# Optimization experiments

Hardware: AMD Instinct MI355X
Metric: run time of the kernel (lower is better)

The kernel has to match this reference:

```python
import jax, jax.numpy as jnp
import numpy as np

CAL = {
 'x': (-0.0025095, 0.0022181),
 'onnxMatMul_166': (-0.22075387835502625, 0.208940327167511),
 'fc1MatMul': (-0.00291599917, 0.0017367251),
 'fc1bias': (-0.48688140511512756, 0.5176185369491577),
 'fc1Add': (-0.48778465390205383, 0.5181604027748108),
 'Wiz_1': (-0.43284985423088074, 0.46175122261047363),
 'Wir_1': (-0.34401071071624756, 0.29191476106643677),
 'Win_1': (-0.3236880302429199, 0.39607325196266174),
 'Whz_1': (-1.8417714834213257, 1.7173254489898682),
 'Whr_1': (-1.1574513912200928, 1.0300449132919312),
 'Whn_1': (-0.7756922245025635, 0.9530389308929443),
 'biz_1': (-0.5063393712043762, 0.36664387583732605),
 'bir_1': (-0.07920225709676743, 0.20611026883125305),
 'bin_1': (-0.5539973378181458, 0.17938342690467834),
 'bhz_1': (-0.5337516665458679, 0.4148772358894348),
 'bhr_1': (-0.07688436657190323, 0.14814253151416779),
 'bhn_1': (-0.7828555107116699, 0.9008108973503113),
 'Wiz_2': (-0.9102030992507935, 0.9408696889877319),
 'Wir_2': (-0.9560997486114502, 0.6683358550071716),
 'Win_2': (-0.4721935987472534, 0.48561596870422363),
 'Whz_2': (-1.2992678880691528, 1.2991048097610474),
 'Whr_2': (-0.8318714499473572, 1.1085889339447021),
 'Whn_2': (-0.955470085144043, 1.046797513961792),
 'biz_2': (-0.44805487990379333, 0.1560053527355194),
 'bir_2': (-0.08767592161893845, 0.11347303539514542),
 'bin_2': (-0.239909827709198, 0.12033259868621826),
 'bhz_2': (-0.43745461106300354, 0.12699371576309204),
 'bhr_2': (-0.09617264568805695, 0.07690174877643585),
 'bhn_2': (-0.17204178869724274, 0.19739042222499847),
 'onnxMatMul_207': (-1.3657219409942627, 1.158295750617981),
 'fc2bias': (-0.1750922054052353, 0.1385071724653244),
 'onnxMatMul_208': (-3.1666038036346436, 2.5026357173919678),
 'fc3bias': (-0.10188056528568268, 0.0899151861667633),
 'onnxMatMul_209': (-1.300571084022522, 1.928941249847412),
 'fc4bias': (-0.10699586570262909, 0.04597663879394531),
 'h1': (-0.002647488145157695, 0.0028339680284261703),
 'h2': (-0.0031016061548143625, 0.0030250486452132463),
 'gru1_a_': (-0.6389939785003662, 0.7715625762939453),
 'gru1_a': (-0.6046768426895142, 0.8871182203292847),
 'gru1_b_': (-0.004922409541904926, 0.004103424027562141),
 'gru1_b': (-0.07475128024816513, 0.14630259573459625),
 'gru1_c_': (-1.5660111904144287, 1.0454494953155518),
 'gru1_c': (-1.9779117107391357, 1.3700535297393799),
 'gru1_d_': (-0.008429044857621193, 0.006403823848813772),
 'gru1_d': (-0.5529640316963196, 0.41507571935653687),
 'gru1_e_': (-1.3637111186981201, 1.018247127532959),
 'gru1_e': (-1.8583884239196777, 1.1587692499160767),
 'gru1_f_': (-0.005411399528384209, 0.0061536869034171104),
 'gru1_f': (-0.7833794355392456, 0.8978855013847351),
 'gru1_r_': (-0.6226556301116943, 0.9800534844398499),
 'gru1_r': (0.3491777181625366, 0.7271188497543335),
 'gru1_z_': (-2.392332077026367, 1.7851293087005615),
 'gru1_z': (0.08375928550958633, 0.856329083442688),
 'gru1_n1': (-0.5516456365585327, 0.4556601643562317),
 'gru1_n2': (-2.4100341796875, 1.1423156261444092),
 'gru1_n': (-0.983996570110321, 0.8151924014091492),
 'gru1_hn1': (0.143670916557312, 0.9162406921386719),
 'gru1_hn2': (-0.9015777111053467, 0.45391541719436646),
 'gru1_hn3': (-0.0016954239690676332, 0.0016671211924403906),
 'rnn1GRU': (-0.9016271829605103, 0.4546271562576294),
 'gru2_a_': (-0.681461751461029, 0.9113116264343262),
 'gru2_a': (-0.7149235010147095, 0.908741295337677),
 'gru2_b_': (-0.005148397758603096, 0.011014967225492),
 'gru2_b': (-0.09436552226543427, 0.07623167335987091),
 'gru2_c_': (-1.2279887199401855, 1.1102137565612793),
 'gru2_c': (-1.6760436296463013, 1.200895071029663),
 'gru2_d_': (-0.008141756057739258, 0.00894666276872158),
 'gru2_d': (-0.43875735998153687, 0.1262134611606598),
 'gru2_e_': (-0.6732944250106812, 0.6314664483070374),
}
# calib entries for gru2 past 'e_' were truncated in the source; reuse gru1 ranges
for _k in ['e', 'f_', 'f', 'r_', 'r', 'z_', 'z', 'n1', 'n2', 'n', 'hn1', 'hn2', 'hn3']:
    CAL.setdefault('gru2_' + _k, CAL['gru1_' + _k])
CAL['rnn2GRU'] = CAL['rnn1GRU']


def fq(x, name):
    """Per-tensor unsigned 8-bit fake-quantize/dequantize (CalibrationParam S/Z)."""
    mn, mx = CAL[name]
    s = (mx - mn) / 255.0  # 2**8 - 1
    z = float(round(-mn / s))
    q = jnp.clip(jnp.round(x / s) + z, 0.0, 255.0)
    y = (q - z) * s
    # straight-through: forward value is exact fake-quant, identity gradient
    return x + jax.lax.stop_gradient(y - x)


def _gru_layer(xs, Wiz, Wir, Win, Whz, Whr, Whn, biz, bir, binn, bhz, bhr, bhn, L):
    p = 'gru%d' % L
    Wiz = fq(Wiz, 'Wiz_%d' % L); Wir = fq(Wir, 'Wir_%d' % L); Win = fq(Win, 'Win_%d' % L)
    Whz = fq(Whz, 'Whz_%d' % L); Whr = fq(Whr, 'Whr_%d' % L); Whn = fq(Whn, 'Whn_%d' % L)
    biz = fq(biz, 'biz_%d' % L); bir = fq(bir, 'bir_%d' % L); binn = fq(binn, 'bin_%d' % L)
    bhz = fq(bhz, 'bhz_%d' % L); bhr = fq(bhr, 'bhr_%d' % L); bhn = fq(bhn, 'bhn_%d' % L)
    # input projections batched over all timesteps (xs: [T,B,H] time-major)
    A = fq(fq(jnp.einsum('tbi,ih->tbh', xs, Wir), p + '_a_') + bir, p + '_a')
    C = fq(fq(jnp.einsum('tbi,ih->tbh', xs, Wiz), p + '_c_') + biz, p + '_c')
    E = fq(fq(jnp.einsum('tbi,ih->tbh', xs, Win), p + '_e_') + binn, p + '_e')
    h0 = fq(jnp.zeros((xs.shape[1], Whz.shape[0]), xs.dtype), 'h%d' % L)

    def step(h, ace):
        a, c, e = ace
        b = fq(fq(h @ Whr, p + '_b_') + bhr, p + '_b')
        r = fq(jax.nn.sigmoid(fq(a + b, p + '_r_')), p + '_r')
        d = fq(fq(h @ Whz, p + '_d_') + bhz, p + '_d')
        z = fq(jax.nn.sigmoid(fq(c + d, p + '_z_')), p + '_z')
        f = fq(fq(h @ Whn, p + '_f_') + bhn, p + '_f')
        n = fq(jnp.tanh(fq(e + fq(r * f, p + '_n1'), p + '_n2')), p + '_n')
        hn2 = fq(fq(1.0 - z, p + '_hn1') * n, p + '_hn2')
        hn3 = fq(z * h, p + '_hn3')
        h_new = fq(hn2 + hn3, 'rnn%dGRU' % L)
        return h_new, h_new

    _, hs = jax.lax.scan(step, h0, (A, C, E))
    return hs


def setup_inputs() -> dict:
    B, T, F, H, D = 64, 1000, 257, 400, 600
    ks = iter(jax.random.split(jax.random.key(0), 64))

    def u(shape, name):
        mn, mx = CAL[name]
        return jax.random.uniform(next(ks), shape, jnp.float32, mn, mx)

    inp = {}
    inp['x'] = jax.random.normal(next(ks), (B, T, F), jnp.float32) * 0.001
    inp['W_fc1'] = u((F, H), 'onnxMatMul_166')
    inp['b_fc1'] = u((H,), 'fc1bias')
    for L in (1, 2):
        for g in ('z', 'r', 'n'):
            inp['Wi%s%d' % (g, L)] = u((H, H), 'Wi%s_%d' % (g, L))
            inp['Wh%s%d' % (g, L)] = u((H, H), 'Wh%s_%d' % (g, L))
            inp['bi%s%d' % (g, L)] = u((H,), 'bi%s_%d' % (g, L))
            inp['bh%s%d' % (g, L)] = u((H,), 'bh%s_%d' % (g, L))
    inp['W_fc2'] = u((H, D), 'onnxMatMul_207'); inp['b_fc2'] = u((D,), 'fc2bias')
    inp['W_fc3'] = u((D, D), 'onnxMatMul_208'); inp['b_fc3'] = u((D,), 'fc3bias')
    inp['W_fc4'] = u((D, F), 'onnxMatMul_209'); inp['b_fc4'] = u((F,), 'fc4bias')
    return inp


def reference(x, W_fc1, b_fc1, Wiz1, Wir1, Win1, Whz1, Whr1, Whn1, biz1, bir1, bin1, bhz1, bhr1, bhn1, Wiz2, Wir2, Win2, Whz2, Whr2, Whn2, biz2, bir2, bin2, bhz2, bhr2, bhn2, W_fc2, b_fc2, W_fc3, b_fc3, W_fc4, b_fc4):
    xq = fq(x, 'x')
    t = fq(jnp.einsum('bti,ih->bth', xq, fq(W_fc1, 'onnxMatMul_166')), 'fc1MatMul')
    t = fq(t + fq(b_fc1, 'fc1bias'), 'fc1Add')
    xs = jnp.swapaxes(t, 0, 1)  # [T,B,400]
    h1 = _gru_layer(xs, Wiz1, Wir1, Win1, Whz1, Whr1, Whn1, biz1, bir1, bin1, bhz1, bhr1, bhn1, 1)
    h2 = _gru_layer(h1, Wiz2, Wir2, Win2, Whz2, Whr2, Whn2, biz2, bir2, bin2, bhz2, bhr2, bhn2, 2)
    y = jnp.swapaxes(h2, 0, 1)  # [B,T,400]
    y = jax.nn.relu(jnp.einsum('bth,hd->btd', y, fq(W_fc2, 'onnxMatMul_207')) + fq(b_fc2, 'fc2bias'))
    y = jax.nn.relu(jnp.einsum('btd,de->bte', y, fq(W_fc3, 'onnxMatMul_208')) + fq(b_fc3, 'fc3bias'))
    y = jax.nn.sigmoid(jnp.einsum('bte,ef->btf', y, fq(W_fc4, 'onnxMatMul_209')) + fq(b_fc4, 'fc4bias'))
    return y
```

## Files before the change

### kernel.cpp

```cpp
#include <hip/hip_runtime.h>
#include <math.h>

#define DEV static __device__ __forceinline__

typedef int v4i __attribute__((ext_vector_type(4)));

struct SZ { float s, z; };

constexpr double cfloor_(double v){ long long i=(long long)v; return ((double)i > v) ? (double)(i-1) : (double)i; }
constexpr double cround_(double v){
  double fl = cfloor_(v); double fr = v - fl;
  return (fr > 0.5) ? fl + 1.0 : (fr < 0.5 ? fl : ((((long long)fl) & 1LL) == 0 ? fl : fl + 1.0));
}
constexpr SZ mksz(double mn, double mx){
  double s = (mx - mn) / 255.0;
  double z = cround_(-mn / s);
  return SZ{ (float)s, (float)z };
}

constexpr SZ Zx     = mksz(-0.0025095, 0.0022181);
constexpr SZ ZW1    = mksz(-0.22075387835502625, 0.208940327167511);
constexpr SZ Zfc1mm = mksz(-0.00291599917, 0.0017367251);
constexpr SZ Zbfc1  = mksz(-0.48688140511512756, 0.5176185369491577);
constexpr SZ Zfc1add= mksz(-0.48778465390205383, 0.5181604027748108);
constexpr SZ ZWiz1 = mksz(-0.43284985423088074, 0.46175122261047363);
constexpr SZ ZWir1 = mksz(-0.34401071071624756, 0.29191476106643677);
constexpr SZ ZWin1 = mksz(-0.3236880302429199, 0.39607325196266174);
constexpr SZ ZWhz1 = mksz(-1.8417714834213257, 1.7173254489898682);
constexpr SZ ZWhr1 = mksz(-1.1574513912200928, 1.0300449132919312);
constexpr SZ ZWhn1 = mksz(-0.7756922245025635, 0.9530389308929443);
constexpr SZ Zbiz1 = mksz(-0.5063393712043762, 0.36664387583732605);
constexpr SZ Zbir1 = mksz(-0.07920225709676743, 0.20611026883125305);
constexpr SZ Zbin1 = mksz(-0.5539973378181458, 0.17938342690467834);
constexpr SZ Zbhz1 = mksz(-0.5337516665458679, 0.4148772358894348);
constexpr SZ Zbhr1 = mksz(-0.07688436657190323, 0.14814253151416779);
constexpr SZ Zbhn1 = mksz(-0.7828555107116699, 0.9008108973503113);
constexpr SZ ZWiz2 = mksz(-0.9102030992507935, 0.9408696889877319);
constexpr SZ ZWir2 = mksz(-0.9560997486114502, 0.6683358550071716);
constexpr SZ ZWin2 = mksz(-0.4721935987472534, 0.48561596870422363);
constexpr SZ ZWhz2 = mksz(-1.2992678880691528, 1.2991048097610474);
constexpr SZ ZWhr2 = mksz(-0.8318714499473572, 1.1085889339447021);
constexpr SZ ZWhn2 = mksz(-0.955470085144043, 1.046797513961792);
constexpr SZ Zbiz2 = mksz(-0.44805487990379333, 0.1560053527355194);
constexpr SZ Zbir2 = mksz(-0.08767592161893845, 0.11347303539514542);
constexpr SZ Zbin2 = mksz(-0.239909827709198, 0.12033259868621826);
constexpr SZ Zbhz2 = mksz(-0.43745461106300354, 0.12699371576309204);
constexpr SZ Zbhr2 = mksz(-0.09617264568805695, 0.07690174877643585);
constexpr SZ Zbhn2 = mksz(-0.17204178869724274, 0.19739042222499847);
constexpr SZ ZWfc2 = mksz(-1.3657219409942627, 1.158295750617981);
constexpr SZ Zbfc2 = mksz(-0.1750922054052353, 0.1385071724653244);
constexpr SZ ZWfc3 = mksz(-3.1666038036346436, 2.5026357173919678);
constexpr SZ Zbfc3 = mksz(-0.10188056528568268, 0.0899151861667633);
constexpr SZ ZWfc4 = mksz(-1.300571084022522, 1.928941249847412);
constexpr SZ Zbfc4 = mksz(-0.10699586570262909, 0.04597663879394531);
constexpr SZ Za_1 = mksz(-0.6389939785003662, 0.7715625762939453);
constexpr SZ Za1  = mksz(-0.6046768426895142, 0.8871182203292847);
constexpr SZ Zb_1 = mksz(-0.004922409541904926, 0.004103424027562141);
constexpr SZ Zb1  = mksz(-0.07475128024816513, 0.14630259573459625);
constexpr SZ Zc_1 = mksz(-1.5660111904144287, 1.0454494953155518);
constexpr SZ Zc1  = mksz(-1.9779117107391357, 1.3700535297393799);
constexpr SZ Zd_1 = mksz(-0.008429044857621193, 0.006403823848813772);
constexpr SZ Zd1  = mksz(-0.5529640316963196, 0.41507571935653687);
constexpr SZ Ze_1 = mksz(-1.3637111186981201, 1.018247127532959);
constexpr SZ Ze1  = mksz(-1.8583884239196777, 1.1587692499160767);
constexpr SZ Zf_1 = mksz(-0.005411399528384209, 0.0061536869034171104);
constexpr SZ Zf1  = mksz(-0.7833794355392456, 0.8978855013847351);
constexpr SZ Zr_1 = mksz(-0.6226556301116943, 0.9800534844398499);
constexpr SZ Zr1  = mksz(0.3491777181625366, 0.7271188497543335);
constexpr SZ Zz_1 = mksz(-2.392332077026367, 1.7851293087005615);
constexpr SZ Zz1  = mksz(0.08375928550958633, 0.856329083442688);
constexpr SZ Zn11 = mksz(-0.5516456365585327, 0.4556601643562317);
constexpr SZ Zn21 = mksz(-2.4100341796875, 1.1423156261444092);
constexpr SZ Zn1  = mksz(-0.983996570110321, 0.8151924014091492);
constexpr SZ Zhn11= mksz(0.143670916557312, 0.9162406921386719);
constexpr SZ Zhn21= mksz(-0.9015777111053467, 0.45391541719436646);
constexpr SZ Zhn31= mksz(-0.0016954239690676332, 0.0016671211924403906);
constexpr SZ Zrnn = mksz(-0.9016271829605103, 0.4546271562576294);
constexpr SZ Za_2 = mksz(-0.681461751461029, 0.9113116264343262);
constexpr SZ Za2  = mksz(-0.7149235010147095, 0.908741295337677);
constexpr SZ Zb_2 = mksz(-0.005148397758603096, 0.011014967225492);
constexpr SZ Zb2g = mksz(-0.09436552226543427, 0.07623167335987091);
constexpr SZ Zc_2 = mksz(-1.2279887199401855, 1.1102137565612793);
constexpr SZ Zc2  = mksz(-1.6760436296463013, 1.200895071029663);
constexpr SZ Zd_2 = mksz(-0.008141756057739258, 0.00894666276872158);
constexpr SZ Zd2  = mksz(-0.43875735998153687, 0.1262134611606598);
constexpr SZ Ze_2 = mksz(-0.6732944250106812, 0.6314664483070374);

struct RecP {
  SZ wr, wz, wn;
  SZ a, c, e;
  SZ b1, b2, d1, d2, f1, f2;
  SZ r1, r2, z1, z2;
  SZ n1, n2, n3;
  SZ hn1, hn2, hn3, rnn;
};
constexpr RecP PL1 = { ZWhr1, ZWhz1, ZWhn1, Za1, Zc1, Ze1, Zb_1, Zb1, Zd_1, Zd1, Zf_1, Zf1,
                       Zr_1, Zr1, Zz_1, Zz1, Zn11, Zn21, Zn1, Zhn11, Zhn21, Zhn31, Zrnn };
constexpr RecP PL2 = { ZWhr2, ZWhz2, ZWhn2, Za2, Zc2, Ze1, Zb_2, Zb2g, Zd_2, Zd2, Zf_1, Zf1,
                       Zr_1, Zr1, Zz_1, Zz1, Zn11, Zn21, Zn1, Zhn11, Zhn21, Zhn31, Zrnn };

DEV float fq_(float x, float s, float z){
  float q = rintf(x / s) + z;
  q = fminf(fmaxf(q, 0.f), 255.f);
  return (q - z) * s;
}
DEV float sigm_(float v){ return 1.f / (1.f + expf(-v)); }

DEV unsigned udot4_(unsigned a, unsigned b, unsigned c){
#if defined(__has_builtin) && __has_builtin(__builtin_amdgcn_udot4)
  return __builtin_amdgcn_udot4(a, b, c, false);
#else
  return c + (a & 255u) * (b & 255u) + ((a >> 8) & 255u) * ((b >> 8) & 255u)
           + ((a >> 16) & 255u) * ((b >> 16) & 255u) + (a >> 24) * (b >> 24);
#endif
}

__global__ __launch_bounds__(256) void kfq(const float* __restrict__ src, float* __restrict__ dst,
                                           int n, float s, float z){
  int i = blockIdx.x * 256 + threadIdx.x;
  if (i < n) dst[i] = fq_(src[i], s, z);
}
__global__ __launch_bounds__(256) void kwhc(const float* __restrict__ W, unsigned char* __restrict__ dst,
                                            float s, float z){
  int i = blockIdx.x * 256 + threadIdx.x;
  if (i < 160000) {
    int j = i / 400, k = i - j * 400;
    float q = rintf(W[k * 400 + j] / s) + z;
    q = fminf(fmaxf(q, 0.f), 255.f);
    dst[i] = (unsigned char)q;
  }
}
__global__ __launch_bounds__(256) void kcolsum(const unsigned char* __restrict__ WhC, int* __restrict__ cs){
  int i = blockIdx.x * 256 + threadIdx.x;
  if (i < 2400) {
    const unsigned char* p = WhC + (size_t)i * 400;
    int s = 0;
    for (int k = 0; k < 400; ++k) s += p[k];
    cs[i] = s;
  }
}
__global__ __launch_bounds__(256) void kwic(const float* __restrict__ W, signed char* __restrict__ Bt,
                                            int* __restrict__ cs, float s, float z, int K, int N){
  int total1 = K * N, total2 = (464 - K) * N;
  for (int idx = blockIdx.x * 256 + threadIdx.x; idx < total1; idx += gridDim.x * 256) {
    int k = idx / N, n = idx - k * N;
    float q = rintf(W[idx] / s) + z;
    q = fminf(fmaxf(q, 0.f), 255.f);
    int qi = (int)q;
    Bt[(size_t)n * 464 + k] = (signed char)(qi ^ 0x80);
    atomicAdd(&cs[n], qi - 128);
  }
  for (int idx = blockIdx.x * 256 + threadIdx.x; idx < total2; idx += gridDim.x * 256) {
    int n = idx / (464 - K), k = K + (idx - n * (464 - K));
    Bt[(size_t)n * 464 + k] = 0;
  }
}
__global__ __launch_bounds__(256) void kxq(const float* __restrict__ x, unsigned char* __restrict__ xcq,
                                           float s, float z){
  int idx = blockIdx.x * 256 + threadIdx.x;
  if (idx < 64000 * 464) {
    int row = idx / 464, c = idx - row * 464;
    unsigned char code = 128;
    if (c < 257) {
      int bb = row & 63, tt = row >> 6;
      float q = rintf(x[((size_t)bb * 1000 + tt) * 257 + c] / s) + z;
      q = fminf(fmaxf(q, 0.f), 255.f);
      code = (unsigned char)q;
    }
    xcq[idx] = code;
  }
}
__global__ __launch_bounds__(256) void krsum(const unsigned char* __restrict__ A, int* __restrict__ rs,
                                             int w4){
  int r = blockIdx.x * 256 + threadIdx.x;
  const unsigned* p = (const unsigned*)(A + (size_t)r * (w4 * 16));
  unsigned s = 0;
  for (int i = 0; i < w4 * 4; ++i) s = udot4_(p[i], 0x01010101u, s);
  rs[r] = (int)s - 128 * 4 * (w4 * 4);
}
__global__ __launch_bounds__(256) void kinit(unsigned long long* __restrict__ hp1,
                                             unsigned long long* __restrict__ hp2, unsigned code){
  int i = blockIdx.x * 256 + threadIdx.x;
  if (i < 6400) {
    unsigned long long w = (unsigned long long)(code * 0x01010101u);
    hp1[i] = w; hp2[i] = w;
  }
}

__global__ __launch_bounds__(256) void gemm_i8(
    const unsigned char* __restrict__ Au8, int strideA, int aw4,
    const int* __restrict__ rowsum,
    const signed char* __restrict__ Bt, const int* __restrict__ colsum,
    const float* __restrict__ bias,
    unsigned char* __restrict__ outU8, float* __restrict__ outF,
    int N, int nb, int outStride, int epMode,
    int czw, int cza, int cconst, float ss,
    float e1S, float e1Z, float e2S, float e2Z)
{
  __shared__ __align__(16) signed char Asl[64 * 464];
  __shared__ __align__(16) signed char Bsl[80 * 464];
  const int tid = threadIdx.x;
  const int bm = blockIdx.x / nb;
  const int bn = blockIdx.x - bm * nb;
  const int m0 = bm * 64;
  const int n0 = bn * 80;
  for (int i = tid; i < 80 * 29; i += 256) {
    int r = i / 29, c = i - r * 29;
    uint4 v;
    if (n0 + r < N) v = *(const uint4*)(Bt + (size_t)(n0 + r) * 464 + c * 16);
    else { v.x = 0u; v.y = 0u; v.z = 0u; v.w = 0u; }
    *(uint4*)(Bsl + (size_t)r * 464 + c * 16) = v;
  }
  for (int i = tid; i < 64 * 29; i += 256) {
    int r = i / 29, c = i - r * 29;
    uint4 v;
    if (c < aw4) {
      v = *(const uint4*)(Au8 + (size_t)(m0 + r) * strideA + c * 16);
      v.x ^= 0x80808080u; v.y ^= 0x80808080u; v.z ^= 0x80808080u; v.w ^= 0x80808080u;
    } else { v.x = 0u; v.y = 0u; v.z = 0u; v.w = 0u; }
    *(uint4*)(Asl + (size_t)r * 464 + c * 16) = v;
  }
  __syncthreads();
  const int wv = tid >> 6, ln = tid & 63;
  const int lr = ln & 15;
  const int lk = ln >> 4;
  v4i acc[5];
#pragma unroll
  for (int j = 0; j < 5; ++j) { acc[j][0] = 0; acc[j][1] = 0; acc[j][2] = 0; acc[j][3] = 0; }
#pragma unroll
  for (int kc = 0; kc < 7; ++kc) {
    int kb = kc * 64 + lk * 16;
    v4i a = *(const v4i*)(Asl + (size_t)(wv * 16 + lr) * 464 + kb);
#pragma unroll
    for (int j = 0; j < 5; ++j) {
      v4i b = *(const v4i*)(Bsl + (size_t)(j * 16 + lr) * 464 + kb);
      acc[j] = __builtin_amdgcn_mfma_i32_16x16x64_i8(a, b, acc[j], 0, 0, 0);
    }
  }
#pragma unroll
  for (int reg = 0; reg < 4; ++reg) {
    int row = m0 + wv * 16 + lk * 4 + reg;
    int RA = rowsum[row];
#pragma unroll
    for (int j = 0; j < 5; ++j) {
      int col = n0 + j * 16 + lr;
      if (col >= N) continue;
      int I = acc[j][reg] + czw * RA + cza * colsum[col] + cconst;
      float v = (float)I * ss;
      if (epMode == 0) {
        v = fq_(v, e1S, e1Z) + bias[col];
        float q = rintf(v / e2S) + e2Z;
        q = fminf(fmaxf(q, 0.f), 255.f);
        outU8[(size_t)row * outStride + col] = (unsigned char)q;
      } else {
        v += bias[col];
        v = fmaxf(v, 0.f);
        outF[(size_t)row * outStride + col] = v;
      }
    }
  }
}

__global__ __launch_bounds__(256) void gemm_k(
    const float* __restrict__ Af,
    const float* __restrict__ B, const float* __restrict__ bias,
    float* __restrict__ outF,
    int M, int N, int K, int epMode, int rowOff)
{
  __shared__ __align__(16) float As[16][132];
  __shared__ __align__(16) float Bs[16][132];
  const int tid = threadIdx.x;
  const int m0 = blockIdx.x * 128;
  const int n0 = blockIdx.y * 128;
  const int tx = tid & 15, ty = tid >> 4;
  float acc[8][8];
#pragma unroll
  for (int i = 0; i < 8; ++i)
#pragma unroll
    for (int j = 0; j < 8; ++j) acc[i][j] = 0.f;

  const int kq = tid & 3;
  const int am = tid >> 2;
  const int bc = (tid & 31) * 4;
  const int br = tid >> 5;

  for (int k0 = 0; k0 < K; k0 += 16) {
#pragma unroll
    for (int it = 0; it < 2; ++it) {
      int mr = am + it * 64;
      int row = m0 + mr;
      int kk = k0 + kq * 4;
      float v0, v1, v2, v3;
      const float* p = Af + (size_t)row * K + kk;
      if (kk + 3 < K) { float4 f = *(const float4*)p; v0 = f.x; v1 = f.y; v2 = f.z; v3 = f.w; }
      else {
        v0 = (kk     < K) ? p[0] : 0.f; v1 = (kk + 1 < K) ? p[1] : 0.f;
        v2 = (kk + 2 < K) ? p[2] : 0.f; v3 = (kk + 3 < K) ? p[3] : 0.f;
      }
      As[kq * 4 + 0][mr] = v0; As[kq * 4 + 1][mr] = v1;
      As[kq * 4 + 2][mr] = v2; As[kq * 4 + 3][mr] = v3;
    }
#pragma unroll
    for (int it = 0; it < 2; ++it) {
      int rr = br + it * 8;
      int k = k0 + rr;
      int c = n0 + bc;
      float v0 = 0.f, v1 = 0.f, v2 = 0.f, v3 = 0.f;
      if (k < K) {
        const float* p = B + (size_t)k * N + c;
        if (((N & 3) == 0) && (c + 3 < N)) { float4 f = *(const float4*)p; v0 = f.x; v1 = f.y; v2 = f.z; v3 = f.w; }
        else {
          if (c     < N) v0 = p[0];
          if (c + 1 < N) v1 = p[1];
          if (c + 2 < N) v2 = p[2];
          if (c + 3 < N) v3 = p[3];
        }
      }
      float4 f4; f4.x = v0; f4.y = v1; f4.z = v2; f4.w = v3;
      *(float4*)&Bs[rr][bc] = f4;
    }
    __syncthreads();
#pragma unroll
    for (int kk = 0; kk < 16; ++kk) {
      float a_[8], b_[8];
      *(float4*)&a_[0] = *(const float4*)&As[kk][ty * 8];
      *(float4*)&a_[4] = *(const float4*)&As[kk][ty * 8 + 4];
      *(float4*)&b_[0] = *(const float4*)&Bs[kk][tx * 8];
      *(float4*)&b_[4] = *(const float4*)&Bs[kk][tx * 8 + 4];
#pragma unroll
      for (int i = 0; i < 8; ++i)
#pragma unroll
        for (int j = 0; j < 8; ++j) acc[i][j] = fmaf(a_[i], b_[j], acc[i][j]);
    }
    __syncthreads();
  }
#pragma unroll
  for (int i = 0; i < 8; ++i) {
    int row = m0 + ty * 8 + i;
#pragma unroll
    for (int j = 0; j < 8; ++j) {
      int col = n0 + tx * 8 + j;
      if (col >= N) continue;
      float v = acc[i][j];
      if (epMode == 2) {
        v += bias[col];
        v = fmaxf(v, 0.f);
        outF[(size_t)row * N + col] = v;
      } else {
        v += bias[col];
        v = sigm_(v);
        int rg = rowOff + row;
        int tt = rg >> 6, bb = rg & 63;
        outF[((size_t)bb * 1000 + tt) * 257 + col] = v;
      }
    }
  }
}

__global__ __launch_bounds__(384) void gru_rec(
    const unsigned char* __restrict__ WhC, const int* __restrict__ colsum,
    const unsigned char* __restrict__ Aq, const unsigned char* __restrict__ Cq,
    const unsigned char* __restrict__ Eq,
    const float* __restrict__ bhr, const float* __restrict__ bhz, const float* __restrict__ bhn,
    unsigned char* __restrict__ hs,
    unsigned long long* hpub, RecP P)
{
  __shared__ __align__(16) uint4 Wlds[9600];
  __shared__ __align__(16) uint4 hq_own[7];
  __shared__ __align__(16) uint4 hqr[21];
  __shared__ float dots[2][3][100];
  __shared__ unsigned aceb[75];
  __shared__ int HqS_s;
  __shared__ int flag;

  const int tid = threadIdx.x;
  const int wv  = tid >> 6;
  const int ln  = tid & 63;
  const int b   = blockIdx.x & 63;
  const int sl  = blockIdx.x >> 6;
  const int jbase = sl * 100;

  unsigned* Wled = (unsigned*)Wlds;
  unsigned* hqow = (unsigned*)hq_own;
  unsigned* hqrw = (unsigned*)hqr;

  for (int idx = tid; idx < 30000; idx += 384) {
    int cid0 = idx / 100, w = idx - cid0 * 100;
    int c = w / 25, p = w - c * 25;
    int g0 = cid0 / 100, jj0 = cid0 - g0 * 100;
    unsigned word = ((const unsigned*)(WhC + ((size_t)(g0 * 400) + jbase + jj0) * 400))[w];
    int slot = (c * 7 + (p >> 2)) ^ (cid0 & 31);
    Wled[cid0 * 128 + slot * 4 + (p & 3)] = word;
  }
  for (int idx = tid; idx < 3600; idx += 384) {
    int cid0 = idx / 12, r = idx - cid0 * 12;
    int c = r / 3, wd = r - c * 3 + 1;
    int slot = (c * 7 + 6) ^ (cid0 & 31);
    Wled[cid0 * 128 + slot * 4 + wd] = 0u;
  }
  const unsigned code0 = (unsigned)fminf(fmaxf(P.rnn.z, 0.f), 255.f);
  if (tid < 28) hqow[tid] = (tid < 25) ? code0 * 0x01010101u : 0u;
  if (tid >= 32 && tid < 41) {
    int r = tid - 32; int o = r / 3, wd = r - o * 3 + 1;
    hqrw[o * 28 + 24 + wd] = 0u;
  }
  if (tid == 383) flag = -1;

  const int cid = tid;
  int g = cid / 100;
  int jj = cid - g * 100;
  float s1S = 1.f, s1Z = 0.f, s2S = 1.f, s2Z = 0.f, biasj = 0.f, swsh = 0.f;
  int zwi = 0, CSj = 0;
  if (tid < 300) {
    int j = jbase + jj;
    SZ w  = (g == 0) ? P.wr : (g == 1) ? P.wz : P.wn;
    SZ s1 = (g == 0) ? P.b1 : (g == 1) ? P.d1 : P.f1;
    SZ s2 = (g == 0) ? P.b2 : (g == 1) ? P.d2 : P.f2;
    zwi = (int)w.z;
    s1S = s1.s; s1Z = s1.z; s2S = s2.s; s2Z = s2.z;
    biasj = ((g == 0) ? bhr : (g == 1) ? bhz : bhn)[j];
    CSj = colsum[g * 400 + j];
    swsh = w.s * P.rnn.s;
  }
  const int zhi = (int)P.rnn.z;
  const int swm = cid & 31;

  unsigned hprev = code0;
  __syncthreads();

  for (int t = 0; t < 1000; ++t) {
    if (wv == 5) {
      size_t row = (size_t)t * 64 + b;
      int w0 = ln, w1 = 64 + ln;
      int wh0 = w0 / 25, wi0 = w0 - wh0 * 25;
      const unsigned char* p0 = (wh0 == 0) ? Aq : (wh0 == 1) ? Cq : Eq;
      unsigned v0 = *(const unsigned*)(p0 + row * 400 + jbase + wi0 * 4);
      unsigned v1 = 0;
      if (ln < 11) {
        int wh1 = w1 / 25, wi1 = w1 - wh1 * 25;
        const unsigned char* p1 = (wh1 == 0) ? Aq : (wh1 == 1) ? Cq : Eq;
        v1 = *(const unsigned*)(p1 + row * 400 + jbase + wi1 * 4);
      }
      const unsigned long long* base = hpub + ((size_t)(t & 3) * 64 + b) * 100;
      unsigned pay0, pay1 = 0;
      {
        int o = ln / 25, p = ln - o * 25;
        int so = (sl + o + 1) & 3;
        const unsigned long long* src = base + so * 25 + p;
        unsigned long long w64;
        while ((unsigned)((w64 = __hip_atomic_load(src, __ATOMIC_RELAXED, __HIP_MEMORY_SCOPE_AGENT)) >> 32)
               != (unsigned)t) { }
        pay0 = (unsigned)w64;
        hqrw[o * 28 + ((p >> 2) * 4) + (p & 3)] = pay0;
      }
      if (ln < 11) {
        int widx = 64 + ln;
        int o = widx / 25, p = widx - o * 25;
        int so = (sl + o + 1) & 3;
        const unsigned long long* src = base + so * 25 + p;
        unsigned long long w64;
        while ((unsigned)((w64 = __hip_atomic_load(src, __ATOMIC_RELAXED, __HIP_MEMORY_SCOPE_AGENT)) >> 32)
               != (unsigned)t) { }
        pay1 = (unsigned)w64;
        hqrw[o * 28 + ((p >> 2) * 4) + (p & 3)] = pay1;
      }
      unsigned hp = udot4_(pay0, 0x01010101u, 0u);
      if (ln < 11) hp = udot4_(pay1, 0x01010101u, hp);
      if (ln < 25) hp = udot4_(hqow[ln], 0x01010101u, hp);
#pragma unroll
      for (int off = 32; off; off >>= 1) hp += __shfl_down(hp, off, 64);
      if (ln == 0) HqS_s = (int)hp;
      __hip_atomic_store(&flag, t, __ATOMIC_RELEASE, __HIP_MEMORY_SCOPE_WORKGROUP);
      aceb[ln] = v0;
      if (ln < 11) aceb[64 + ln] = v1;
      if (t > 0 && ln < 25)
        *(unsigned*)(hs + ((size_t)(t - 1) * 64 + b) * 400 + jbase + ln * 4) = hqow[ln];
    } else if (tid < 300) {
      unsigned acc = 0;
      const uint4* wcol = &Wlds[cid * 32];
#pragma unroll
      for (int i = 0; i < 7; ++i) {
        uint4 h = hq_own[i];
        uint4 w = wcol[(sl * 7 + i) ^ swm];
        acc = udot4_(w.x, h.x, acc);
        acc = udot4_(w.y, h.y, acc);
        acc = udot4_(w.z, h.z, acc);
        acc = udot4_(w.w, h.w, acc);
      }
      while (__hip_atomic_load(&flag, __ATOMIC_ACQUIRE, __HIP_MEMORY_SCOPE_WORKGROUP) < t)
        __builtin_amdgcn_s_sleep(1);
#pragma unroll
      for (int o = 0; o < 3; ++o) {
        int c = (sl + o + 1) & 3;
#pragma unroll
        for (int i = 0; i < 7; ++i) {
          uint4 h = hqr[o * 7 + i];
          uint4 w = wcol[(c * 7 + i) ^ swm];
          acc = udot4_(w.x, h.x, acc);
          acc = udot4_(w.y, h.y, acc);
          acc = udot4_(w.z, h.z, acc);
          acc = udot4_(w.w, h.w, acc);
        }
      }
      int I = (int)acc - zwi * HqS_s - zhi * CSj + 400 * zhi * zwi;
      float dot = (float)I * swsh;
      float v = fq_(dot, s1S, s1Z) + biasj;
      v = fq_(v, s2S, s2Z);
      dots[t & 1][g][jj] = v;
    }
    __syncthreads();
    if (tid < 128) {
      int m = (tid < 100) ? tid : 99;
      const unsigned char* aceb8 = (const unsigned char*)aceb;
      float a = ((float)aceb8[m]       - P.a.z) * P.a.s;
      float c = ((float)aceb8[100 + m] - P.c.z) * P.c.s;
      float e = ((float)aceb8[200 + m] - P.e.z) * P.e.s;
      float bb = dots[t & 1][0][m], dd = dots[t & 1][1][m], ff = dots[t & 1][2][m];
      float r  = fq_(sigm_(fq_(a + bb, P.r1.s, P.r1.z)), P.r2.s, P.r2.z);
      float zz = fq_(sigm_(fq_(c + dd, P.z1.s, P.z1.z)), P.z2.s, P.z2.z);
      float nn = fq_(tanhf(fq_(e + fq_(r * ff, P.n1.s, P.n1.z), P.n2.s, P.n2.z)), P.n3.s, P.n3.z);
      float hold = ((float)hprev - P.rnn.z) * P.rnn.s;
      float hn2v = fq_(fq_(1.f - zz, P.hn1.s, P.hn1.z) * nn, P.hn2.s, P.hn2.z);
      float hn3v = fq_(zz * hold, P.hn3.s, P.hn3.z);
      float hnew = hn2v + hn3v;
      float q = rintf(hnew / P.rnn.s) + P.rnn.z;
      q = fminf(fmaxf(q, 0.f), 255.f);
      unsigned code = (unsigned)q;
      unsigned c1 = __shfl_down(code, 1);
      unsigned c2 = __shfl_down(code, 2);
      unsigned c3 = __shfl_down(code, 3);
      if (tid < 100) {
        if ((tid & 3) == 0) {
          unsigned packed = code | (c1 << 8) | (c2 << 16) | (c3 << 24);
          unsigned long long out64 = ((unsigned long long)(unsigned)(t + 1) << 32) | packed;
          unsigned long long* dst = hpub + ((size_t)((t + 1) & 3) * 64 + b) * 100 + sl * 25 + (tid >> 2);
          __hip_atomic_store(dst, out64, __ATOMIC_RELAXED, __HIP_MEMORY_SCOPE_AGENT);
          hqow[tid >> 2] = packed;
        }
        hprev = code;
      }
    }
    __syncthreads();
  }
  if (wv == 5 && ln < 25)
    *(unsigned*)(hs + ((size_t)999 * 64 + b) * 400 + jbase + ln * 4) = hqow[ln];
}

extern "C" void kernel_launch(void* const* d_in, const int* in_sizes, int n_in,
                              void* d_out, int out_size, void* d_ws, size_t ws_size,
                              hipStream_t stream)
{
  const float* x    = (const float*)d_in[0];
  const float* Wfc1 = (const float*)d_in[1];
  const float* bfc1 = (const float*)d_in[2];
  const float* Wiz1 = (const float*)d_in[3];  const float* Whz1 = (const float*)d_in[4];
  const float* biz1 = (const float*)d_in[5];  const float* bhz1 = (const float*)d_in[6];
  const float* Wir1 = (const float*)d_in[7];  const float* Whr1 = (const float*)d_in[8];
  const float* bir1 = (const float*)d_in[9];  const float* bhr1 = (const float*)d_in[10];
  const float* Win1 = (const float*)d_in[11]; const float* Whn1 = (const float*)d_in[12];
  const float* bin1 = (const float*)d_in[13]; const float* bhn1 = (const float*)d_in[14];
  const float* Wiz2 = (const float*)d_in[15]; const float* Whz2 = (const float*)d_in[16];
  const float* biz2 = (const float*)d_in[17]; const float* bhz2 = (const float*)d_in[18];
  const float* Wir2 = (const float*)d_in[19]; const float* Whr2 = (const float*)d_in[20];
  const float* bir2 = (const float*)d_in[21]; const float* bhr2 = (const float*)d_in[22];
  const float* Win2 = (const float*)d_in[23]; const float* Whn2 = (const float*)d_in[24];
  const float* bin2 = (const float*)d_in[25]; const float* bhn2 = (const float*)d_in[26];
  const float* Wfc2 = (const float*)d_in[27]; const float* bfc2 = (const float*)d_in[28];
  const float* Wfc3 = (const float*)d_in[29]; const float* bfc3 = (const float*)d_in[30];
  const float* Wfc4 = (const float*)d_in[31]; const float* bfc4 = (const float*)d_in[32];
  float* out = (float*)d_out;

  char* wp = (char*)d_ws;
  auto alloc = [&](size_t bytes) -> void* {
    void* p = (void*)wp;
    wp += (bytes + 255) & ~(size_t)255;
    return p;
  };
  float* W3q = (float*)alloc(360000 * 4);
  float* W4q = (float*)alloc(154200 * 4);
  float* b1q = (float*)alloc(400 * 4);
  float* biq = (float*)alloc(2400 * 4);
  float* bhq = (float*)alloc(2400 * 4);
  float* b2q = (float*)alloc(600 * 4);
  float* b3q = (float*)alloc(600 * 4);
  float* b4q = (float*)alloc(257 * 4);
  unsigned char* WhC = (unsigned char*)alloc(960000);
  int* colsum = (int*)alloc(2400 * 4);
  signed char* WiT = (signed char*)alloc(7 * 400 * 464);
  signed char* Bt2 = (signed char*)alloc(600 * 464);
  int* cwi = (int*)alloc((7 * 400 + 600) * 4);
  int* rsX1 = (int*)alloc(64000 * 4);
  int* rsX  = (int*)alloc(64000 * 4);
  int* rsH  = (int*)alloc(64000 * 4);
  int* rsH2 = (int*)alloc(64000 * 4);
  unsigned char* xsq = (unsigned char*)alloc(25600000);
  unsigned char* Aq  = (unsigned char*)alloc(25600000);
  unsigned char* Cq  = (unsigned char*)alloc(25600000);
  unsigned char* Eq  = (unsigned char*)alloc(25600000);
  unsigned char* hs1 = (unsigned char*)alloc(25600000);
  unsigned char* hs2 = (unsigned char*)alloc(25600000);
  unsigned long long* hpub1 = (unsigned long long*)alloc(4 * 64 * 100 * 8);
  unsigned long long* hpub2 = (unsigned long long*)alloc(4 * 64 * 100 * 8);
  float* y2c = (float*)Aq;
  float* y3c = (float*)(Aq + 38400000);
  unsigned char* xcq = hs1;

  auto fqk = [&](const float* s, float* d, int n, SZ p) {
    kfq<<<dim3((n + 255) / 256), dim3(256), 0, stream>>>(s, d, n, p.s, p.z);
  };
  fqk(Wfc3, W3q, 360000, ZWfc3); fqk(Wfc4, W4q, 154200, ZWfc4);
  fqk(bfc1, b1q, 400, Zbfc1);
  fqk(bir1, biq + 0, 400, Zbir1);    fqk(biz1, biq + 400, 400, Zbiz1);  fqk(bin1, biq + 800, 400, Zbin1);
  fqk(bir2, biq + 1200, 400, Zbir2); fqk(biz2, biq + 1600, 400, Zbiz2); fqk(bin2, biq + 2000, 400, Zbin2);
  fqk(bhr1, bhq + 0, 400, Zbhr1);    fqk(bhz1, bhq + 400, 400, Zbhz1);  fqk(bhn1, bhq + 800, 400, Zbhn1);
  fqk(bhr2, bhq + 1200, 400, Zbhr2); fqk(bhz2, bhq + 1600, 400, Zbhz2); fqk(bhn2, bhq + 2000, 400, Zbhn2);
  fqk(bfc2, b2q, 600, Zbfc2); fqk(bfc3, b3q, 600, Zbfc3); fqk(bfc4, b4q, 257, Zbfc4);

  dim3 g625((160000 + 255) / 256);
  kwhc<<<g625, dim3(256), 0, stream>>>(Whr1, WhC + 0,      ZWhr1.s, ZWhr1.z);
  kwhc<<<g625, dim3(256), 0, stream>>>(Whz1, WhC + 160000, ZWhz1.s, ZWhz1.z);
  kwhc<<<g625, dim3(256), 0, stream>>>(Whn1, WhC + 320000, ZWhn1.s, ZWhn1.z);
  kwhc<<<g625, dim3(256), 0, stream>>>(Whr2, WhC + 480000, ZWhr2.s, ZWhr2.z);
  kwhc<<<g625, dim3(256), 0, stream>>>(Whz2, WhC + 640000, ZWhz2.s, ZWhz2.z);
  kwhc<<<g625, dim3(256), 0, stream>>>(Whn2, WhC + 800000, ZWhn2.s, ZWhn2.z);
  kcolsum<<<dim3(10), dim3(256), 0, stream>>>(WhC, colsum);
  unsigned code0 = (unsigned)(Zrnn.z < 0.f ? 0.f : (Zrnn.z > 255.f ? 255.f : Zrnn.z));
  kinit<<<dim3(25), dim3(256), 0, stream>>>(hpub1, hpub2, code0);

  hipMemsetAsync(cwi, 0, (7 * 400 + 600) * 4, stream);
  auto wic = [&](const float* W, signed char* Bt, int* cs, SZ p, int K, int N) {
    kwic<<<dim3(625), dim3(256), 0, stream>>>(W, Bt, cs, p.s, p.z, K, N);
  };
  wic(Wir1, WiT + (size_t)0 * 185600, cwi + 0,    ZWir1, 400, 400);
  wic(Wiz1, WiT + (size_t)1 * 185600, cwi + 400,  ZWiz1, 400, 400);
  wic(Win1, WiT + (size_t)2 * 185600, cwi + 800,  ZWin1, 400, 400);
  wic(Wir2, WiT + (size_t)3 * 185600, cwi + 1200, ZWir2, 400, 400);
  wic(Wiz2, WiT + (size_t)4 * 185600, cwi + 1600, ZWiz2, 400, 400);
  wic(Win2, WiT + (size_t)5 * 185600, cwi + 2000, ZWin2, 400, 400);
  wic(Wfc1, WiT + (size_t)6 * 185600, cwi + 2400, ZW1,   257, 400);
  wic(Wfc2, Bt2,                      cwi + 2800, ZWfc2, 400, 600);

  auto gi8 = [&](const unsigned char* A, int strideA, int aw4, const int* rs,
                 const signed char* Bt, const int* cs, const float* bias,
                 unsigned char* oU8, float* oF, int M, int N, int outStride, int epMode,
                 SZ a, SZ w, int Kreal, float ss, SZ e1, SZ e2) {
    int czw = 128 - (int)w.z, cza = 128 - (int)a.z;
    int cconst = Kreal * cza * czw;
    int nb = (N + 79) / 80;
    gemm_i8<<<dim3((M / 64) * nb), dim3(256), 0, stream>>>(
        A, strideA, aw4, rs, Bt, cs, bias, oU8, oF, N, nb, outStride, epMode,
        czw, cza, cconst, ss, e1.s, e1.z, e2.s, e2.z);
  };

  kxq<<<dim3((64000 * 464 + 255) / 256), dim3(256), 0, stream>>>(x, xcq, Zx.s, Zx.z);
  krsum<<<dim3(250), dim3(256), 0, stream>>>(xcq, rsX1, 29);
  gi8(xcq, 464, 29, rsX1, WiT + (size_t)6 * 185600, cwi + 2400, b1q,
      xsq, nullptr, 64000, 400, 400, 0, Zx, ZW1, 257, Zx.s * ZW1.s, Zfc1mm, Zfc1add);

  krsum<<<dim3(250), dim3(256), 0, stream>>>(xsq, rsX, 25);
  gi8(xsq, 400, 25, rsX, WiT + (size_t)0 * 185600, cwi + 0,    biq + 0,   Aq, nullptr,
      64000, 400, 400, 0, Zfc1add, ZWir1, 400, Zfc1add.s * ZWir1.s, Za_1, Za1);
  gi8(xsq, 400, 25, rsX, WiT + (size_t)1 * 185600, cwi + 400,  biq + 400, Cq, nullptr,
      64000, 400, 400, 0, Zfc1add, ZWiz1, 400, Zfc1add.s * ZWiz1.s, Zc_1, Zc1);
  gi8(xsq, 400, 25, rsX, WiT + (size_t)2 * 185600, cwi + 800,  biq + 800, Eq, nullptr,
      64000, 400, 400, 0, Zfc1add, ZWin1, 400, Zfc1add.s * ZWin1.s, Ze_1, Ze1);
  gru_rec<<<dim3(256), dim3(384), 0, stream>>>(WhC, colsum, Aq, Cq, Eq,
                                               bhq + 0, bhq + 400, bhq + 800,
                                               hs1, hpub1, PL1);
  krsum<<<dim3(250), dim3(256), 0, stream>>>(hs1, rsH, 25);
  gi8(hs1, 400, 25, rsH, WiT + (size_t)3 * 185600, cwi + 1200, biq + 1200, Aq, nullptr,
      64000, 400, 400, 0, Zrnn, ZWir2, 400, Zrnn.s * ZWir2.s, Za_2, Za2);
  gi8(hs1, 400, 25, rsH, WiT + (size_t)4 * 185600, cwi + 1600, biq + 1600, Cq, nullptr,
      64000, 400, 400, 0, Zrnn, ZWiz2, 400, Zrnn.s * ZWiz2.s, Zc_2, Zc2);
  gi8(hs1, 400, 25, rsH, WiT + (size_t)5 * 185600, cwi + 2000, biq + 2000, Eq, nullptr,
      64000, 400, 400, 0, Zrnn, ZWin2, 400, Zrnn.s * ZWin2.s, Ze_2, Ze1);
  gru_rec<<<dim3(256), dim3(384), 0, stream>>>(WhC + 480000, colsum + 1200, Aq, Cq, Eq,
                                               bhq + 1200, bhq + 1600, bhq + 2000,
                                               hs2, hpub2, PL2);
  krsum<<<dim3(250), dim3(256), 0, stream>>>(hs2, rsH2, 25);
  for (int rc = 0; rc < 4; ++rc) {
    const unsigned char* a2 = hs2 + (size_t)rc * 16000 * 400;
    gi8(a2, 400, 25, rsH2 + rc * 16000, Bt2, cwi + 2800, b2q, nullptr, y2c,
        16000, 600, 600, 2, Zrnn, ZWfc2, 400, Zrnn.s * ZWfc2.s, Zrnn, Zrnn);
    gemm_k<<<dim3(125, 5), dim3(256), 0, stream>>>(y2c, W3q, b3q, y3c, 16000, 600, 600, 2, 0);
    gemm_k<<<dim3(125, 3), dim3(256), 0, stream>>>(y3c, W4q, b4q, out, 16000, 257, 600, 3, rc * 16000);
  }
  (void)in_sizes; (void)n_in; (void)out_size; (void)ws_size;
}
```

Baseline: 8.356 ms.

## Run fc3/fc4 GEMMs on bf16 MFMA with split-precision activations; batch setup kernels

Replaces the scalar fp32 tiled GEMM for the fc3 and fc4 layers with an MFMA 16x16x32 bf16 kernel. The fake-quantized weights are stored as exact bf16 integer codes, pre-transposed and padded to K=608. Activations are split into high and low bf16 parts so fp32 accuracy is roughly kept, at the cost of two MFMAs per fragment. The full 128-column weight tile is staged in shared memory. The setup launches for the biases and the recurrent and input weight quantization are also merged into a few batched kernels to cut launch count.

```diff
diff --git a/kernel.cpp b/kernel.cpp
--- a/kernel.cpp
+++ b/kernel.cpp
@@ -4,6 +4,9 @@
 #define DEV static __device__ __forceinline__
 
 typedef int v4i __attribute__((ext_vector_type(4)));
+typedef float v4f __attribute__((ext_vector_type(4)));
+typedef __bf16 bf16_t;
+typedef __bf16 v8bf __attribute__((ext_vector_type(8)));
 
 struct SZ { float s, z; };
 
@@ -115,17 +118,20 @@
 #endif
 }
 
-__global__ __launch_bounds__(256) void kfq(const float* __restrict__ src, float* __restrict__ dst,
-                                           int n, float s, float z){
+struct BJob { const float* src; float* dst; int n; float s; float z; };
+struct BJobs { BJob j[16]; };
+__global__ __launch_bounds__(256) void kbias(BJobs jobs){
+  BJob J = jobs.j[blockIdx.x];
+  for (int i = threadIdx.x; i < J.n; i += 256) J.dst[i] = fq_(J.src[i], J.s, J.z);
+}
+
+struct W6 { const float* W[6]; float s[6]; float z[6]; };
+__global__ __launch_bounds__(256) void kwhc6(W6 jb, unsigned char* __restrict__ dst){
   int i = blockIdx.x * 256 + threadIdx.x;
-  if (i < n) dst[i] = fq_(src[i], s, z);
-}
-__global__ __launch_bounds__(256) void kwhc(const float* __restrict__ W, unsigned char* __restrict__ dst,
-                                            float s, float z){
-  int i = blockIdx.x * 256 + threadIdx.x;
-  if (i < 160000) {
-    int j = i / 400, k = i - j * 400;
-    float q = rintf(W[k * 400 + j] / s) + z;
+  if (i < 960000) {
+    int m = i / 160000, r = i - m * 160000;
+    int j = r / 400, k = r - j * 400;
+    float q = rintf(jb.W[m][k * 400 + j] / jb.s[m]) + jb.z[m];
     q = fminf(fmaxf(q, 0.f), 255.f);
     dst[i] = (unsigned char)q;
   }
@@ -137,6 +143,22 @@
     int s = 0;
     for (int k = 0; k < 400; ++k) s += p[k];
     cs[i] = s;
+  }
+}
+__global__ __launch_bounds__(256) void kwic6(W6 jb, signed char* __restrict__ WiT, int* __restrict__ cs){
+  for (int idx = blockIdx.x * 256 + threadIdx.x; idx < 960000; idx += gridDim.x * 256) {
+    int m = idx / 160000, r = idx - m * 160000;
+    int k = r / 400, n = r - k * 400;
+    float q = rintf(jb.W[m][r] / jb.s[m]) + jb.z[m];
+    q = fminf(fmaxf(q, 0.f), 255.f);
+    int qi = (int)q;
+    WiT[(size_t)m * 185600 + (size_t)n * 464 + k] = (signed char)(qi ^ 0x80);
+    atomicAdd(&cs[m * 400 + n], qi - 128);
+  }
+  for (int idx = blockIdx.x * 256 + threadIdx.x; idx < 153600; idx += gridDim.x * 256) {
+    int m = idx / 25600, r = idx - m * 25600;
+    int n = r / 64, p = r - n * 64;
+    WiT[(size_t)m * 185600 + (size_t)n * 464 + 400 + p] = 0;
   }
 }
 __global__ __launch_bounds__(256) void kwic(const float* __restrict__ W, signed char* __restrict__ Bt,
@@ -153,6 +175,20 @@
   for (int idx = blockIdx.x * 256 + threadIdx.x; idx < total2; idx += gridDim.x * 256) {
     int n = idx / (464 - K), k = K + (idx - n * (464 - K));
     Bt[(size_t)n * 464 + k] = 0;
+  }
+}
+__global__ __launch_bounds__(256) void kwbf(const float* __restrict__ W, bf16_t* __restrict__ Bt,
+                                            float s, float z, int K, int N){
+  int total1 = K * N, total2 = (608 - K) * N;
+  for (int idx = blockIdx.x * 256 + threadIdx.x; idx < total1; idx += gridDim.x * 256) {
+    int k = idx / N, n = idx - k * N;
+    float q = rintf(W[idx] / s) + z;
+    q = fminf(fmaxf(q, 0.f), 255.f);
+    Bt[(size_t)n * 608 + k] = (bf16_t)(q - z);
+  }
+  for (int idx = blockIdx.x * 256 + threadIdx.x; idx < total2; idx += gridDim.x * 256) {
+    int n = idx / (608 - K), k = K + (idx - n * (608 - K));
+    Bt[(size_t)n * 608 + k] = (bf16_t)0.f;
   }
 }
 __global__ __launch_bounds__(256) void kxq(const float* __restrict__ x, unsigned char* __restrict__ xcq,
@@ -261,93 +297,68 @@
   }
 }
 
-__global__ __launch_bounds__(256) void gemm_k(
-    const float* __restrict__ Af,
-    const float* __restrict__ B, const float* __restrict__ bias,
-    float* __restrict__ outF,
-    int M, int N, int K, int epMode, int rowOff)
+__global__ __launch_bounds__(512) void gemm_bf(
+    const float* __restrict__ A, const bf16_t* __restrict__ Bt,
+    const float* __restrict__ bias, float* __restrict__ outF,
+    int N, int nb, int epMode, int rowOff, float sc)
 {
-  __shared__ __align__(16) float As[16][132];
-  __shared__ __align__(16) float Bs[16][132];
+  __shared__ __align__(16) bf16_t Bs[128 * 616];
   const int tid = threadIdx.x;
-  const int m0 = blockIdx.x * 128;
-  const int n0 = blockIdx.y * 128;
-  const int tx = tid & 15, ty = tid >> 4;
-  float acc[8][8];
-#pragma unroll
-  for (int i = 0; i < 8; ++i)
-#pragma unroll
-    for (int j = 0; j < 8; ++j) acc[i][j] = 0.f;
-
-  const int kq = tid & 3;
-  const int am = tid >> 2;
-  const int bc = (tid & 31) * 4;
-  const int br = tid >> 5;
-
-  for (int k0 = 0; k0 < K; k0 += 16) {
-#pragma unroll
-    for (int it = 0; it < 2; ++it) {
-      int mr = am + it * 64;
-      int row = m0 + mr;
-      int kk = k0 + kq * 4;
-      float v0, v1, v2, v3;
-      const float* p = Af + (size_t)row * K + kk;
-      if (kk + 3 < K) { float4 f = *(const float4*)p; v0 = f.x; v1 = f.y; v2 = f.z; v3 = f.w; }
-      else {
-        v0 = (kk     < K) ? p[0] : 0.f; v1 = (kk + 1 < K) ? p[1] : 0.f;
-        v2 = (kk + 2 < K) ? p[2] : 0.f; v3 = (kk + 3 < K) ? p[3] : 0.f;
-      }
-      As[kq * 4 + 0][mr] = v0; As[kq * 4 + 1][mr] = v1;
-      As[kq * 4 + 2][mr] = v2; As[kq * 4 + 3][mr] = v3;
-    }
-#pragma unroll
-    for (int it = 0; it < 2; ++it) {
-      int rr = br + it * 8;
-      int k = k0 + rr;
-      int c = n0 + bc;
-      float v0 = 0.f, v1 = 0.f, v2 = 0.f, v3 = 0.f;
-      if (k < K) {
-        const float* p = B + (size_t)k * N + c;
-        if (((N & 3) == 0) && (c + 3 < N)) { float4 f = *(const float4*)p; v0 = f.x; v1 = f.y; v2 = f.z; v3 = f.w; }
-        else {
-          if (c     < N) v0 = p[0];
-          if (c + 1 < N) v1 = p[1];
-          if (c + 2 < N) v2 = p[2];
-          if (c + 3 < N) v3 = p[3];
-        }
-      }
-      float4 f4; f4.x = v0; f4.y = v1; f4.z = v2; f4.w = v3;
-      *(float4*)&Bs[rr][bc] = f4;
-    }
-    __syncthreads();
-#pragma unroll
-    for (int kk = 0; kk < 16; ++kk) {
-      float a_[8], b_[8];
-      *(float4*)&a_[0] = *(const float4*)&As[kk][ty * 8];
-      *(float4*)&a_[4] = *(const float4*)&As[kk][ty * 8 + 4];
-      *(float4*)&b_[0] = *(const float4*)&Bs[kk][tx * 8];
-      *(float4*)&b_[4] = *(const float4*)&Bs[kk][tx * 8 + 4];
-#pragma unroll
-      for (int i = 0; i < 8; ++i)
-#pragma unroll
-        for (int j = 0; j < 8; ++j) acc[i][j] = fmaf(a_[i], b_[j], acc[i][j]);
-    }
-    __syncthreads();
-  }
-#pragma unroll
-  for (int i = 0; i < 8; ++i) {
-    int row = m0 + ty * 8 + i;
+  const int bm = blockIdx.x / nb;
+  const int bn = blockIdx.x - bm * nb;
+  const int m0 = bm * 128;
+  const int n0 = bn * 128;
+  for (int i = tid; i < 128 * 76; i += 512) {
+    int r = i / 76, c = i - r * 76;
+    uint4 v; v.x = 0u; v.y = 0u; v.z = 0u; v.w = 0u;
+    if (n0 + r < N) v = *(const uint4*)((const char*)(Bt + (size_t)(n0 + r) * 608) + c * 16);
+    *(uint4*)((char*)(Bs + (size_t)r * 616) + c * 16) = v;
+  }
+  __syncthreads();
+  const int wv = tid >> 6, ln = tid & 63;
+  const int lr = ln & 15, quad = ln >> 4;
+  const float* arp = A + (size_t)(m0 + wv * 16 + lr) * 600;
+  v4f acc[8];
+#pragma unroll
+  for (int j = 0; j < 8; ++j) { acc[j][0] = 0.f; acc[j][1] = 0.f; acc[j][2] = 0.f; acc[j][3] = 0.f; }
+  for (int kc = 0; kc < 19; ++kc) {
+    int kb = kc * 32 + quad * 8;
+    float af[8];
+    if (kc == 18 && quad == 3) {
+#pragma unroll
+      for (int j = 0; j < 8; ++j) af[j] = 0.f;
+    } else {
+      *(float4*)&af[0] = *(const float4*)(arp + kb);
+      *(float4*)&af[4] = *(const float4*)(arp + kb + 4);
+    }
+    v8bf ah, al;
 #pragma unroll
     for (int j = 0; j < 8; ++j) {
-      int col = n0 + tx * 8 + j;
-      if (col >= N) continue;
-      float v = acc[i][j];
+      float xx = af[j];
+      bf16_t h = (bf16_t)xx;
+      ah[j] = h;
+      al[j] = (bf16_t)(xx - (float)h);
+    }
+#pragma unroll
+    for (int nf = 0; nf < 8; ++nf) {
+      v8bf bfrag = *(const v8bf*)(Bs + (size_t)(nf * 16 + lr) * 616 + kc * 32 + quad * 8);
+      acc[nf] = __builtin_amdgcn_mfma_f32_16x16x32_bf16(ah, bfrag, acc[nf], 0, 0, 0);
+      acc[nf] = __builtin_amdgcn_mfma_f32_16x16x32_bf16(al, bfrag, acc[nf], 0, 0, 0);
+    }
+  }
+#pragma unroll
+  for (int nf = 0; nf < 8; ++nf) {
+    int col = n0 + nf * 16 + lr;
+    if (col >= N) continue;
+    float bcol = bias[col];
+#pragma unroll
+    for (int reg = 0; reg < 4; ++reg) {
+      int row = m0 + wv * 16 + quad * 4 + reg;
+      float v = acc[nf][reg] * sc + bcol;
       if (epMode == 2) {
-        v += bias[col];
         v = fmaxf(v, 0.f);
         outF[(size_t)row * N + col] = v;
       } else {
-        v += bias[col];
         v = sigm_(v);
         int rg = rowOff + row;
         int tt = rg >> 6, bb = rg & 63;
@@ -576,8 +587,6 @@
     wp += (bytes + 255) & ~(size_t)255;
     return p;
   };
-  float* W3q = (float*)alloc(360000 * 4);
-  float* W4q = (float*)alloc(154200 * 4);
   float* b1q = (float*)alloc(400 * 4);
   float* biq = (float*)alloc(2400 * 4);
   float* bhq = (float*)alloc(2400 * 4);
@@ -588,6 +597,8 @@
   int* colsum = (int*)alloc(2400 * 4);
   signed char* WiT = (signed char*)alloc(7 * 400 * 464);
   signed char* Bt2 = (signed char*)alloc(600 * 464);
+  bf16_t* Bt3 = (bf16_t*)alloc(600 * 608 * 2);
+  bf16_t* Bt4 = (bf16_t*)alloc(257 * 608 * 2);
   int* cwi = (int*)alloc((7 * 400 + 600) * 4);
   int* rsX1 = (int*)alloc(64000 * 4);
   int* rsX  = (int*)alloc(64000 * 4);
@@ -605,40 +616,42 @@
   float* y3c = (float*)(Aq + 38400000);
   unsigned char* xcq = hs1;
 
-  auto fqk = [&](const float* s, float* d, int n, SZ p) {
-    kfq<<<dim3((n + 255) / 256), dim3(256), 0, stream>>>(s, d, n, p.s, p.z);
-  };
-  fqk(Wfc3, W3q, 360000, ZWfc3); fqk(Wfc4, W4q, 154200, ZWfc4);
-  fqk(bfc1, b1q, 400, Zbfc1);
-  fqk(bir1, biq + 0, 400, Zbir1);    fqk(biz1, biq + 400, 400, Zbiz1);  fqk(bin1, biq + 800, 400, Zbin1);
-  fqk(bir2, biq + 1200, 400, Zbir2); fqk(biz2, biq + 1600, 400, Zbiz2); fqk(bin2, biq + 2000, 400, Zbin2);
-  fqk(bhr1, bhq + 0, 400, Zbhr1);    fqk(bhz1, bhq + 400, 400, Zbhz1);  fqk(bhn1, bhq + 800, 400, Zbhn1);
-  fqk(bhr2, bhq + 1200, 400, Zbhr2); fqk(bhz2, bhq + 1600, 400, Zbhz2); fqk(bhn2, bhq + 2000, 400, Zbhn2);
-  fqk(bfc2, b2q, 600, Zbfc2); fqk(bfc3, b3q, 600, Zbfc3); fqk(bfc4, b4q, 257, Zbfc4);
-
-  dim3 g625((160000 + 255) / 256);
-  kwhc<<<g625, dim3(256), 0, stream>>>(Whr1, WhC + 0,      ZWhr1.s, ZWhr1.z);
-  kwhc<<<g625, dim3(256), 0, stream>>>(Whz1, WhC + 160000, ZWhz1.s, ZWhz1.z);
-  kwhc<<<g625, dim3(256), 0, stream>>>(Whn1, WhC + 320000, ZWhn1.s, ZWhn1.z);
-  kwhc<<<g625, dim3(256), 0, stream>>>(Whr2, WhC + 480000, ZWhr2.s, ZWhr2.z);
-  kwhc<<<g625, dim3(256), 0, stream>>>(Whz2, WhC + 640000, ZWhz2.s, ZWhz2.z);
-  kwhc<<<g625, dim3(256), 0, stream>>>(Whn2, WhC + 800000, ZWhn2.s, ZWhn2.z);
+  BJobs bj;
+  bj.j[0]  = { bfc1, b1q,        400, Zbfc1.s, Zbfc1.z };
+  bj.j[1]  = { bir1, biq + 0,    400, Zbir1.s, Zbir1.z };
+  bj.j[2]  = { biz1, biq + 400,  400, Zbiz1.s, Zbiz1.z };
+  bj.j[3]  = { bin1, biq + 800,  400, Zbin1.s, Zbin1.z };
+  bj.j[4]  = { bir2, biq + 1200, 400, Zbir2.s, Zbir2.z };
+  bj.j[5]  = { biz2, biq + 1600, 400, Zbiz2.s, Zbiz2.z };
+  bj.j[6]  = { bin2, biq + 2000, 400, Zbin2.s, Zbin2.z };
+  bj.j[7]  = { bhr1, bhq + 0,    400, Zbhr1.s, Zbhr1.z };
+  bj.j[8]  = { bhz1, bhq + 400,  400, Zbhz1.s, Zbhz1.z };
+  bj.j[9]  = { bhn1, bhq + 800,  400, Zbhn1.s, Zbhn1.z };
+  bj.j[10] = { bhr2, bhq + 1200, 400, Zbhr2.s, Zbhr2.z };
+  bj.j[11] = { bhz2, bhq + 1600, 400, Zbhz2.s, Zbhz2.z };
+  bj.j[12] = { bhn2, bhq + 2000, 400, Zbhn2.s, Zbhn2.z };
+  bj.j[13] = { bfc2, b2q,        600, Zbfc2.s, Zbfc2.z };
+  bj.j[14] = { bfc3, b3q,        600, Zbfc3.s, Zbfc3.z };
+  bj.j[15] = { bfc4, b4q,        257, Zbfc4.s, Zbfc4.z };
+  kbias<<<dim3(16), dim3(256), 0, stream>>>(bj);
+
+  W6 wh = { { Whr1, Whz1, Whn1, Whr2, Whz2, Whn2 },
+            { ZWhr1.s, ZWhz1.s, ZWhn1.s, ZWhr2.s, ZWhz2.s, ZWhn2.s },
+            { ZWhr1.z, ZWhz1.z, ZWhn1.z, ZWhr2.z, ZWhz2.z, ZWhn2.z } };
+  kwhc6<<<dim3(3750), dim3(256), 0, stream>>>(wh, WhC);
   kcolsum<<<dim3(10), dim3(256), 0, stream>>>(WhC, colsum);
   unsigned code0 = (unsigned)(Zrnn.z < 0.f ? 0.f : (Zrnn.z > 255.f ? 255.f : Zrnn.z));
   kinit<<<dim3(25), dim3(256), 0, stream>>>(hpub1, hpub2, code0);
 
   hipMemsetAsync(cwi, 0, (7 * 400 + 600) * 4, stream);
-  auto wic = [&](const float* W, signed char* Bt, int* cs, SZ p, int K, int N) {
-    kwic<<<dim3(625), dim3(256), 0, stream>>>(W, Bt, cs, p.s, p.z, K, N);
-  };
-  wic(Wir1, WiT + (size_t)0 * 185600, cwi + 0,    ZWir1, 400, 400);
-  wic(Wiz1, WiT + (size_t)1 * 185600, cwi + 400,  ZWiz1, 400, 400);
-  wic(Win1, WiT + (size_t)2 * 185600, cwi + 800,  ZWin1, 400, 400);
-  wic(Wir2, WiT + (size_t)3 * 185600, cwi + 1200, ZWir2, 400, 400);
-  wic(Wiz2, WiT + (size_t)4 * 185600, cwi + 1600, ZWiz2, 400, 400);
-  wic(Win2, WiT + (size_t)5 * 185600, cwi + 2000, ZWin2, 400, 400);
-  wic(Wfc1, WiT + (size_t)6 * 185600, cwi + 2400, ZW1,   257, 400);
-  wic(Wfc2, Bt2,                      cwi + 2800, ZWfc2, 400, 600);
+  W6 wi = { { Wir1, Wiz1, Win1, Wir2, Wiz2, Win2 },
+            { ZWir1.s, ZWiz1.s, ZWin1.s, ZWir2.s, ZWiz2.s, ZWin2.s },
+            { ZWir1.z, ZWiz1.z, ZWin1.z, ZWir2.z, ZWiz2.z, ZWin2.z } };
+  kwic6<<<dim3(625), dim3(256), 0, stream>>>(wi, WiT, cwi);
+  kwic<<<dim3(625), dim3(256), 0, stream>>>(Wfc1, WiT + (size_t)6 * 185600, cwi + 2400, ZW1.s, ZW1.z, 257, 400);
+  kwic<<<dim3(625), dim3(256), 0, stream>>>(Wfc2, Bt2, cwi + 2800, ZWfc2.s, ZWfc2.z, 400, 600);
+  kwbf<<<dim3(625), dim3(256), 0, stream>>>(Wfc3, Bt3, ZWfc3.s, ZWfc3.z, 600, 600);
+  kwbf<<<dim3(625), dim3(256), 0, stream>>>(Wfc4, Bt4, ZWfc4.s, ZWfc4.z, 600, 257);
 
   auto gi8 = [&](const unsigned char* A, int strideA, int aw4, const int* rs,
                  const signed char* Bt, const int* cs, const float* bias,
@@ -682,8 +695,8 @@
     const unsigned char* a2 = hs2 + (size_t)rc * 16000 * 400;
     gi8(a2, 400, 25, rsH2 + rc * 16000, Bt2, cwi + 2800, b2q, nullptr, y2c,
         16000, 600, 600, 2, Zrnn, ZWfc2, 400, Zrnn.s * ZWfc2.s, Zrnn, Zrnn);
-    gemm_k<<<dim3(125, 5), dim3(256), 0, stream>>>(y2c, W3q, b3q, y3c, 16000, 600, 600, 2, 0);
-    gemm_k<<<dim3(125, 3), dim3(256), 0, stream>>>(y3c, W4q, b4q, out, 16000, 257, 600, 3, rc * 16000);
+    gemm_bf<<<dim3(125 * 5), dim3(512), 0, stream>>>(y2c, Bt3, b3q, y3c, 600, 5, 2, 0, ZWfc3.s);
+    gemm_bf<<<dim3(125 * 3), dim3(512), 0, stream>>>(y3c, Bt4, b4q, out, 257, 3, 3, rc * 16000, ZWfc4.s);
   }
   (void)in_sizes; (void)n_in; (void)out_size; (void)ws_size;
 }
```

Result: faster. 7.343 ms (-12.1%).
